# Performance work log

Measured on AMD Instinct MI355X. Metric: run time of the kernel, lower is better.

The kernel has to match this reference:

```python
import jax, jax.numpy as jnp
import numpy as np

D = 64      # in_feats
OUT = 64    # out_feats
MEM = 4     # mem_size
NREL = 8    # num_rels
N = 20000   # num nodes
E = 50000   # num edges
FF = 16     # dim_feedforward (hardcoded in module)
NH = 4      # nhead (hardcoded)
EPS = 1e-5  # LayerNorm eps (torch default)


def _ln(x, w, b):
    m = x.mean(-1, keepdims=True)
    v = ((x - m) ** 2).mean(-1, keepdims=True)
    return (x - m) * jax.lax.rsqrt(v + EPS) * w + b


def _enc(x, Wqkv, bqkv, Wo, bo, W1, b1, W2, b2, ln1w, ln1b, ln2w, ln2b):
    # torch TransformerEncoderLayer, batch_first, post-norm, eval mode, no padding mask (all-zero mask)
    B, S, d = x.shape
    dh = d // NH
    qkv = x @ Wqkv.T + bqkv
    q, k, v = jnp.split(qkv, 3, axis=-1)
    q = q.reshape(B, S, NH, dh)
    k = k.reshape(B, S, NH, dh)
    v = v.reshape(B, S, NH, dh)
    att = jax.nn.softmax(jnp.einsum('bqhd,bkhd->bhqk', q, k) / jnp.sqrt(jnp.float32(dh)), axis=-1)
    o = jnp.einsum('bhqk,bkhd->bqhd', att, v).reshape(B, S, d) @ Wo.T + bo
    x = _ln(x + o, ln1w, ln1b)
    ff = jax.nn.relu(x @ W1.T + b1) @ W2.T + b2
    return _ln(x + ff, ln2w, ln2b)


def setup_inputs() -> dict:
    key = jax.random.key(0)
    ks = jax.random.split(key, 16)
    s = 0.05
    inp = {
        'feat': jax.random.normal(ks[0], (N, D), jnp.float32),
        'src_idx': jax.random.randint(ks[1], (E,), 0, N),
        'dst_idx': jax.random.randint(ks[2], (E,), 0, N),
        'etype': jax.random.randint(ks[3], (E,), 0, NREL),
        'Wqkv': jax.random.normal(ks[4], (3 * D, D), jnp.float32) * s,
        'bqkv': jnp.zeros((3 * D,), jnp.float32),
        'Wo': jax.random.normal(ks[5], (D, D), jnp.float32) * s,
        'bo': jnp.zeros((D,), jnp.float32),
        'W1': jax.random.normal(ks[6], (FF, D), jnp.float32) * s,
        'b1': jnp.zeros((FF,), jnp.float32),
        'W2': jax.random.normal(ks[7], (D, FF), jnp.float32) * s,
        'b2': jnp.zeros((D,), jnp.float32),
        'ln1w': jnp.ones((D,), jnp.float32),
        'ln1b': jnp.zeros((D,), jnp.float32),
        'ln2w': jnp.ones((D,), jnp.float32),
        'ln2b': jnp.zeros((D,), jnp.float32),
        'Wc': jax.random.normal(ks[8], (MEM, D), jnp.float32) * s,
        'bc': jnp.zeros((MEM,), jnp.float32),
        'CLS': jax.random.normal(ks[9], (MEM, D), jnp.float32),
        'SEP': jax.random.normal(ks[10], (D,), jnp.float32),
        'Wm': jax.random.normal(ks[11], (OUT * D, D), jnp.float32) * s,
        'h_bias': jnp.zeros((OUT,), jnp.float32),
    }
    return inp


def reference(feat, src_idx, dst_idx, etype, Wqkv, bqkv, Wo, bo, W1, b1, W2, b2,
              ln1w, ln1b, ln2w, ln2b, Wc, bc, CLS, SEP, Wm, h_bias):
    enc_args = (Wqkv, bqkv, Wo, bo, W1, b1, W2, b2, ln1w, ln1b, ln2w, ln2b)

    def cls_pass(s_, d_):
        # run the shared encoder MEM times with a different CLS token; the math
        # is identical for every relation type, so no per-etype partition needed
        B = s_.shape[0]
        outs = []
        mem = jnp.zeros((B, D), s_.dtype)
        for i in range(MEM):
            cls = jnp.broadcast_to(CLS[i], (B, D))[:, None, :]
            sep = jnp.broadcast_to(SEP, (B, D))[:, None, :]
            seq = jnp.concatenate([cls, s_[:, None, :], sep, d_[:, None, :]], axis=1)  # [B,4,D]
            t = _enc(seq, *enc_args)[:, 0, :]
            outs.append(t)
            mem = mem + t
        return mem, jnp.stack(outs)  # [B,D], [MEM,B,D]

    src = feat[src_idx]  # [E,D]
    dst = feat[dst_idx]
    mem_emb, tmps = cls_pass(src, dst)
    cat_all = tmps @ Wc.T + bc               # [MEM,E,MEM]
    w = (mem_emb @ Wm.T).reshape(E, OUT, D)  # per-edge hypernetwork weight
    msg = jnp.einsum('eoi,ei->eo', w, src)   # [E,OUT]

    # dgl fn.mean aggregation over destination nodes (0 for isolated nodes)
    cnt = jax.ops.segment_sum(jnp.ones((E,), msg.dtype), dst_idx, num_segments=N)
    agg = jax.ops.segment_sum(msg, dst_idx, num_segments=N)
    node_rep = jnp.where(cnt[:, None] > 0, agg / jnp.maximum(cnt, 1.0)[:, None], 0.0)
    node_rep = node_rep + h_bias

    # self loop (same hypernetwork path over every node)
    mem_s, _ = cls_pass(feat, feat)
    hs = (mem_s @ Wm.T).reshape(N, OUT, D)
    node_rep = node_rep + jnp.einsum('noi,ni->no', hs, feat)

    # reconstruct torch concat order of category/label: outer loop etype, inner loop mem idx
    et = etype.astype(jnp.int32)
    counts = jax.ops.segment_sum(jnp.ones((E,), jnp.int32), etype, num_segments=NREL)
    start = jnp.concatenate([jnp.zeros((1,), jnp.int32), jnp.cumsum(counts)[:-1].astype(jnp.int32)])
    order = jnp.argsort(etype, stable=True)
    rank = jnp.zeros((E,), jnp.int32).at[order].set(jnp.arange(E, dtype=jnp.int32) - start[et[order]])
    base = start[et] * MEM + rank                                            # [E]
    pos = base[None, :] + jnp.arange(MEM, dtype=jnp.int32)[:, None] * counts[et][None, :]  # [MEM,E]
    category = jnp.zeros((MEM * E, MEM), cat_all.dtype).at[pos.reshape(-1)].set(cat_all.reshape(-1, MEM))
    label = jnp.zeros((MEM * E,), jnp.int32).at[pos.reshape(-1)].set(
        jnp.repeat(jnp.arange(MEM, dtype=jnp.int32), E))
    return node_rep, label, category
```

## Files before the change

kernel.cpp:

```cpp
#include <hip/hip_runtime.h>
#include <hip/hip_bf16.h>

typedef float f32x4_t __attribute__((ext_vector_type(4)));
typedef short bf16x8_t __attribute__((ext_vector_type(8)));

#define MFMA(a, b, c) __builtin_amdgcn_mfma_f32_16x16x32_bf16(a, b, c, 0, 0, 0)

#define C_Q0   0
#define C_S00  256
#define C_S02  272
#define C_VCLS 288
#define C_VSEP 544

__device__ __forceinline__ short f2bf(float x) {
    return (short)__builtin_bit_cast(unsigned short, __float2bfloat16(x));
}
__device__ __forceinline__ float bf2f(short s) {
    return __builtin_bit_cast(float, ((unsigned)(unsigned short)s) << 16);
}
__device__ __forceinline__ float head_sum16(float v) {
#pragma unroll
    for (int off = 1; off < 16; off <<= 1) v += __shfl_xor(v, off, 64);
    return v;
}

__global__ void k_prep(const float* __restrict__ Wo, const float* __restrict__ Wqkv,
                       const float* __restrict__ W1, const float* __restrict__ W2,
                       const float* __restrict__ Wm, const float* __restrict__ Wc,
                       const float* __restrict__ bqkv,
                       const float* __restrict__ CLS, const float* __restrict__ SEP,
                       const int* __restrict__ etype, const int* __restrict__ dst,
                       short* __restrict__ Bpack, short* __restrict__ WoP,
                       short* __restrict__ WkvP, short* __restrict__ W1P,
                       short* __restrict__ W2P, short* __restrict__ WcP,
                       float* __restrict__ consts,
                       short* __restrict__ WqkP, float* __restrict__ bqk,
                       int* __restrict__ hist, int* __restrict__ cnt, int E)
{
    int bx = blockIdx.x;
    if (bx < 136) {
        int tid = bx * 256 + threadIdx.x;
        short tmp[8];
        if (tid < 32768) {
            int u = tid, lane = u & 63, nt = (u >> 6) & 3, kstep = u >> 8;
            int o = nt * 16 + (lane & 15);
            int kb = kstep * 32 + (lane >> 4) * 8;
#pragma unroll
            for (int t = 0; t < 8; t++) { int k = kb + t; tmp[t] = f2bf(Wm[(o * 64 + (k >> 6)) * 64 + (k & 63)]); }
            *(bf16x8_t*)&Bpack[(size_t)u * 8] = *(bf16x8_t*)tmp;
        } else if (tid < 33280) {
            int u = tid - 32768, lane = u & 63, nt = (u >> 6) & 3, kstep = u >> 8;
            int o = nt * 16 + (lane & 15), kb = kstep * 32 + (lane >> 4) * 8;
#pragma unroll
            for (int t = 0; t < 8; t++) tmp[t] = f2bf(Wo[o * 64 + kb + t]);
            *(bf16x8_t*)&WoP[(size_t)u * 8] = *(bf16x8_t*)tmp;
        } else if (tid < 34304) {
            int u = tid - 33280, lane = u & 63, nt = (u >> 6) & 7, kstep = u >> 9;
            int col = nt * 16 + (lane & 15), kb = kstep * 32 + (lane >> 4) * 8;
            int row = 64 + col;
#pragma unroll
            for (int t = 0; t < 8; t++) tmp[t] = f2bf(Wqkv[row * 64 + kb + t]);
            *(bf16x8_t*)&WkvP[(size_t)u * 8] = *(bf16x8_t*)tmp;
        } else if (tid < 34432) {
            int u = tid - 34304, lane = u & 63, kstep = u >> 6;
            int f = lane & 15, kb = kstep * 32 + (lane >> 4) * 8;
#pragma unroll
            for (int t = 0; t < 8; t++) tmp[t] = f2bf(W1[f * 64 + kb + t]);
            *(bf16x8_t*)&W1P[(size_t)u * 8] = *(bf16x8_t*)tmp;
        } else if (tid < 34688) {
            int u = tid - 34432, lane = u & 63, nt = u >> 6;
            int o = nt * 16 + (lane & 15), kb = (lane >> 4) * 8;
#pragma unroll
            for (int t = 0; t < 8; t++) { int k = kb + t; tmp[t] = (k < 16) ? f2bf(W2[o * 16 + k]) : (short)0; }
            *(bf16x8_t*)&W2P[(size_t)u * 8] = *(bf16x8_t*)tmp;
        } else if (tid < 34816) {
            int u = tid - 34688, lane = u & 63, kstep = u >> 6;
            int m = lane & 15, kb = kstep * 32 + (lane >> 4) * 8;
#pragma unroll
            for (int t = 0; t < 8; t++) tmp[t] = (m < 4) ? f2bf(Wc[m * 64 + kb + t]) : (short)0;
            *(bf16x8_t*)&WcP[(size_t)u * 8] = *(bf16x8_t*)tmp;
        }
    } else if (bx == 136) {
        if (threadIdx.x < 64) {
            int lane = threadIdx.x;
            float ksep = bqkv[64 + lane], vsep = bqkv[128 + lane];
            for (int c = 0; c < 64; c++) {
                float sc = SEP[c];
                ksep += Wqkv[(64 + lane) * 64 + c] * sc;
                vsep += Wqkv[(128 + lane) * 64 + c] * sc;
            }
            consts[C_VSEP + lane] = vsep;
            for (int i = 0; i < 4; i++) {
                float q0 = bqkv[lane], kcls = bqkv[64 + lane], vcls = bqkv[128 + lane];
                for (int c = 0; c < 64; c++) {
                    float cc = CLS[i * 64 + c];
                    q0   += Wqkv[lane * 64 + c] * cc;
                    kcls += Wqkv[(64 + lane) * 64 + c] * cc;
                    vcls += Wqkv[(128 + lane) * 64 + c] * cc;
                }
                consts[C_Q0 + i * 64 + lane] = q0;
                consts[C_VCLS + i * 64 + lane] = vcls;
                float p00 = head_sum16(q0 * kcls) * 0.25f;
                float p02 = head_sum16(q0 * ksep) * 0.25f;
                if ((lane & 15) == 0) {
                    consts[C_S00 + i * 4 + (lane >> 4)] = p00;
                    consts[C_S02 + i * 4 + (lane >> 4)] = p02;
                }
            }
        }
    } else if (bx == 137) {
        __shared__ float q0s[4][64];
        __shared__ float wqk[16][64];
        int tid = threadIdx.x;
        {
            int i = tid >> 6, c = tid & 63;
            float q0 = bqkv[c];
            for (int c2 = 0; c2 < 64; c2++)
                q0 += Wqkv[c * 64 + c2] * CLS[i * 64 + c2];
            q0s[i][c] = q0;
        }
        __syncthreads();
#pragma unroll
        for (int q = 0; q < 4; q++) {
            int idx = tid * 4 + q;
            int ih = idx >> 6, k = idx & 63;
            int ii = ih & 3, hh = ih >> 2;
            float s = 0.f;
#pragma unroll
            for (int u = 0; u < 16; u++)
                s += q0s[ii][hh * 16 + u] * Wqkv[(64 + hh * 16 + u) * 64 + k];
            wqk[ih][k] = 0.25f * s;
        }
        __syncthreads();
        if (tid < 128) {
            int kstep = tid >> 6, lane = tid & 63;
            short tmp[8];
#pragma unroll
            for (int t = 0; t < 8; t++)
                tmp[t] = f2bf(wqk[lane & 15][kstep * 32 + (lane >> 4) * 8 + t]);
            *(bf16x8_t*)&WqkP[(size_t)(kstep * 64 + lane) * 8] = *(bf16x8_t*)tmp;
        } else if (tid < 144) {
            int ihh = tid - 128, ii = ihh & 3, hh = ihh >> 2;
            float s = 0.f;
#pragma unroll
            for (int u = 0; u < 16; u++)
                s += q0s[ii][hh * 16 + u] * bqkv[64 + hh * 16 + u];
            bqk[ihh] = 0.25f * s;
        }
    } else {
        __shared__ int h[8];
        int chunk = bx - 138;
        int tid = threadIdx.x;
        if (tid < 8) h[tid] = 0;
        __syncthreads();
        int e = chunk * 256 + tid;
        if (e < E) {
            atomicAdd(&h[etype[e]], 1);
            atomicAdd(&cnt[dst[e]], 1);
        }
        __syncthreads();
        if (tid < 8) hist[chunk * 8 + tid] = h[tid];
    }
}

__global__ __launch_bounds__(256) void k_kv(const float* __restrict__ feat,
        const short* __restrict__ WkvP, const short* __restrict__ WqkP,
        const float* __restrict__ bqkv, const float* __restrict__ bqk,
        float* __restrict__ vnode, float* __restrict__ qs, int N,
        const int* __restrict__ hist, int* __restrict__ chunkoff,
        int* __restrict__ startg, int* __restrict__ countsg, int nch, int KB)
{
    if ((int)blockIdx.x == KB) {
        if (threadIdx.x < 64) {
            int lane = threadIdx.x;
            int g = lane & 7, seg = lane >> 3;
            int per = (nch + 7) / 8;
            int c0 = seg * per, c1 = c0 + per; if (c1 > nch) c1 = nch;
            int sum = 0;
            for (int c = c0; c < c1; c++) sum += hist[c * 8 + g];
            int pre = 0, tot = 0;
#pragma unroll
            for (int s2 = 0; s2 < 8; s2++) {
                int v = __shfl(sum, s2 * 8 + g, 64);
                tot += v;
                if (s2 < seg) pre += v;
            }
            int run = pre;
            for (int c = c0; c < c1; c++) { chunkoff[c * 8 + g] = run; run += hist[c * 8 + g]; }
            if (seg == 0) {
                countsg[g] = tot;
                int sg = 0;
#pragma unroll
                for (int g2 = 0; g2 < 8; g2++) { int v = __shfl(tot, g2, 64); if (g2 < g) sg += v; }
                startg[g] = sg;
            }
        }
        return;
    }
    __shared__ __align__(16) short sA[64 * 72];
    int tid = threadIdx.x, lane = tid & 63, w = tid >> 6;
    int l15 = lane & 15, lh = lane >> 4;
    int base = blockIdx.x * 64;
#pragma unroll
    for (int rr = 0; rr < 16; rr++) {
        int row = w * 16 + rr;
        int n = base + row; n = n < N ? n : N - 1;
        sA[row * 72 + lane] = f2bf(feat[(size_t)n * 64 + lane]);
    }
    __syncthreads();
    const bf16x8_t* bp = (const bf16x8_t*)WkvP;
    bf16x8_t bv0 = bp[(0 * 8 + 4 + w) * 64 + lane];
    bf16x8_t bv1 = bp[(1 * 8 + 4 + w) * 64 + lane];
    bf16x8_t bq0 = ((const bf16x8_t*)WqkP)[lane];
    bf16x8_t bq1 = ((const bf16x8_t*)WqkP)[64 + lane];
    int kof = lh * 8;
    int col = w * 16 + l15;
    float biasv = bqkv[128 + col];
    float bqv = bqk[l15];
#pragma unroll
    for (int rt = 0; rt < 4; rt++) {
        bf16x8_t a0 = *(const bf16x8_t*)&sA[(rt * 16 + l15) * 72 + kof];
        bf16x8_t a1 = *(const bf16x8_t*)&sA[(rt * 16 + l15) * 72 + 32 + kof];
        f32x4_t av = {0.f, 0.f, 0.f, 0.f};
        av = MFMA(a0, bv0, av); av = MFMA(a1, bv1, av);
#pragma unroll
        for (int r = 0; r < 4; r++) {
            int n = base + rt * 16 + lh * 4 + r;
            if (n < N) vnode[(size_t)n * 64 + col] = av[r] + biasv;
        }
        if (w == 0) {
            f32x4_t aq = {0.f, 0.f, 0.f, 0.f};
            aq = MFMA(a0, bq0, aq); aq = MFMA(a1, bq1, aq);
#pragma unroll
            for (int r = 0; r < 4; r++) {
                int n = base + rt * 16 + lh * 4 + r;
                if (n < N) qs[(size_t)n * 16 + l15] = aq[r] + bqv;
            }
        }
    }
}

struct EncW {
    const float* consts; const float* CLS; const float* bo;
    const float* b1; const float* b2;
    const float* ln1w; const float* ln1b; const float* ln2w; const float* ln2b;
    const short* WoP; const short* W1P; const short* W2P; const short* WcP;
    const float* bc;
};

__global__ __launch_bounds__(256) void k_enc(const int* __restrict__ src_idx,
        const int* __restrict__ dst_idx,
        const float* __restrict__ vnode, const float* __restrict__ qs, EncW W,
        float* __restrict__ mem_out, float* __restrict__ cat_out, int E, int M)
{
    __shared__ __align__(16) short sA[64 * 72];
    __shared__ __align__(16) short sF[64 * 40];
    int tid = threadIdx.x, lane = tid & 63, w = tid >> 6;
    int l15 = lane & 15, lh = lane >> 4;
    int base = blockIdx.x * 16;

#pragma unroll
    for (int z = 0; z < 4; z++) {
        int zz = z * 64 + lane;
        sF[(w * 16 + (zz >> 4)) * 40 + 16 + (zz & 15)] = 0;
    }

    float attc[4], esum0[4];
#pragma unroll
    for (int i = 0; i < 4; i++) {
        float e0 = __expf(W.consts[C_S00 + i * 4 + lh]);
        float e2 = __expf(W.consts[C_S02 + i * 4 + lh]);
        attc[i]  = e0 * W.consts[C_VCLS + i * 64 + lane] + e2 * W.consts[C_VSEP + lane];
        esum0[i] = e0 + e2;
    }

#pragma unroll
    for (int el = 0; el < 4; el++) {
        int eloc = w * 4 + el;
        int ge = base + eloc; int gc = ge < M ? ge : M - 1;
        int s, d;
        if (gc < E) { s = src_idx[gc]; d = dst_idx[gc]; }
        else        { s = gc - E; d = s; }
        float vs_ = vnode[(size_t)s * 64 + lane];
        float vd  = vnode[(size_t)d * 64 + lane];
        float4 qh_s = *(const float4*)&qs[(size_t)s * 16 + lh * 4];
        float4 qh_d = *(const float4*)&qs[(size_t)d * 16 + lh * 4];
        float qsv[4] = {qh_s.x, qh_s.y, qh_s.z, qh_s.w};
        float qdv[4] = {qh_d.x, qh_d.y, qh_d.z, qh_d.w};
#pragma unroll
        for (int i = 0; i < 4; i++) {
            float e1 = __expf(qsv[i]), e3 = __expf(qdv[i]);
            float inv = 1.0f / (esum0[i] + e1 + e3);
            float att = (attc[i] + e1 * vs_ + e3 * vd) * inv;
            sA[(eloc * 4 + i) * 72 + lane] = f2bf(att);
        }
    }

    int arow = (w * 16 + l15) * 72;
    int kof = lh * 8;

    const bf16x8_t* bpo = (const bf16x8_t*)W.WoP;
    f32x4_t ac0 = {0.f,0.f,0.f,0.f}, ac1 = ac0, ac2 = ac0, ac3 = ac0;
#pragma unroll
    for (int kstep = 0; kstep < 2; kstep++) {
        bf16x8_t a = *(const bf16x8_t*)&sA[arow + kstep * 32 + kof];
        ac0 = MFMA(a, bpo[(kstep * 4 + 0) * 64 + lane], ac0);
        ac1 = MFMA(a, bpo[(kstep * 4 + 1) * 64 + lane], ac1);
        ac2 = MFMA(a, bpo[(kstep * 4 + 2) * 64 + lane], ac2);
        ac3 = MFMA(a, bpo[(kstep * 4 + 3) * 64 + lane], ac3);
    }

    float x[4][4], y[4][4];
#pragma unroll
    for (int r = 0; r < 4; r++) { x[0][r] = ac0[r]; x[1][r] = ac1[r]; x[2][r] = ac2[r]; x[3][r] = ac3[r]; }
    float lw1[4], lb1[4];
#pragma unroll
    for (int nt = 0; nt < 4; nt++) {
        float b = W.bo[nt * 16 + l15];
        lw1[nt] = W.ln1w[nt * 16 + l15]; lb1[nt] = W.ln1b[nt * 16 + l15];
#pragma unroll
        for (int r = 0; r < 4; r++) x[nt][r] += b + W.CLS[r * 64 + nt * 16 + l15];
    }
#pragma unroll
    for (int r = 0; r < 4; r++) {
        float sm = head_sum16(x[0][r] + x[1][r] + x[2][r] + x[3][r]);
        float mu = sm * 0.015625f;
        float vv = 0.f;
#pragma unroll
        for (int nt = 0; nt < 4; nt++) { float dd = x[nt][r] - mu; vv = fmaf(dd, dd, vv); }
        vv = head_sum16(vv);
        float rs = rsqrtf(vv * 0.015625f + 1e-5f);
#pragma unroll
        for (int nt = 0; nt < 4; nt++) y[nt][r] = (x[nt][r] - mu) * rs * lw1[nt] + lb1[nt];
    }
#pragma unroll
    for (int nt = 0; nt < 4; nt++)
#pragma unroll
        for (int r = 0; r < 4; r++)
            sA[(w * 16 + lh * 4 + r) * 72 + nt * 16 + l15] = f2bf(y[nt][r]);

    const bf16x8_t* bp1 = (const bf16x8_t*)W.W1P;
    f32x4_t fa = {0.f,0.f,0.f,0.f};
#pragma unroll
    for (int kstep = 0; kstep < 2; kstep++) {
        bf16x8_t a = *(const bf16x8_t*)&sA[arow + kstep * 32 + kof];
        fa = MFMA(a, bp1[kstep * 64 + lane], fa);
    }
    float b1v = W.b1[l15];
#pragma unroll
    for (int r = 0; r < 4; r++)
        sF[(w * 16 + lh * 4 + r) * 40 + l15] = f2bf(fmaxf(fa[r] + b1v, 0.f));

    const bf16x8_t* bp2 = (const bf16x8_t*)W.W2P;
    bf16x8_t af = *(const bf16x8_t*)&sF[(w * 16 + l15) * 40 + kof];
    f32x4_t z0 = {0.f,0.f,0.f,0.f}, z1 = z0, z2 = z0, z3 = z0;
    z0 = MFMA(af, bp2[0 * 64 + lane], z0);
    z1 = MFMA(af, bp2[1 * 64 + lane], z1);
    z2 = MFMA(af, bp2[2 * 64 + lane], z2);
    z3 = MFMA(af, bp2[3 * 64 + lane], z3);

    float t[4][4];
#pragma unroll
    for (int r = 0; r < 4; r++) { x[0][r] = z0[r]; x[1][r] = z1[r]; x[2][r] = z2[r]; x[3][r] = z3[r]; }
    float lw2[4], lb2[4];
#pragma unroll
    for (int nt = 0; nt < 4; nt++) {
        float b = W.b2[nt * 16 + l15];
        lw2[nt] = W.ln2w[nt * 16 + l15]; lb2[nt] = W.ln2b[nt * 16 + l15];
#pragma unroll
        for (int r = 0; r < 4; r++) x[nt][r] += b + y[nt][r];
    }
#pragma unroll
    for (int r = 0; r < 4; r++) {
        float sm = head_sum16(x[0][r] + x[1][r] + x[2][r] + x[3][r]);
        float mu = sm * 0.015625f;
        float vv = 0.f;
#pragma unroll
        for (int nt = 0; nt < 4; nt++) { float dd = x[nt][r] - mu; vv = fmaf(dd, dd, vv); }
        vv = head_sum16(vv);
        float rs = rsqrtf(vv * 0.015625f + 1e-5f);
#pragma unroll
        for (int nt = 0; nt < 4; nt++) t[nt][r] = (x[nt][r] - mu) * rs * lw2[nt] + lb2[nt];
    }

    int eloc = w * 4 + lh, ge = base + eloc;

    if (base < E) {
#pragma unroll
        for (int nt = 0; nt < 4; nt++)
#pragma unroll
            for (int r = 0; r < 4; r++)
                sA[(w * 16 + lh * 4 + r) * 72 + nt * 16 + l15] = f2bf(t[nt][r]);
        const bf16x8_t* bpc = (const bf16x8_t*)W.WcP;
        f32x4_t ca = {0.f,0.f,0.f,0.f};
#pragma unroll
        for (int kstep = 0; kstep < 2; kstep++) {
            bf16x8_t a = *(const bf16x8_t*)&sA[arow + kstep * 32 + kof];
            ca = MFMA(a, bpc[kstep * 64 + lane], ca);
        }
        if (l15 < 4 && ge < E) {
            float bcv = W.bc[l15];
#pragma unroll
            for (int r = 0; r < 4; r++)
                cat_out[((size_t)r * E + ge) * 4 + l15] = ca[r] + bcv;
        }
    }

    if (ge < M) {
#pragma unroll
        for (int nt = 0; nt < 4; nt++)
            mem_out[(size_t)ge * 64 + nt * 16 + l15] = t[nt][0] + t[nt][1] + t[nt][2] + t[nt][3];
    }
}

__global__ __launch_bounds__(256, 3) void k_hyper(
        const float* __restrict__ feat, const int* __restrict__ src_idx,
        const int* __restrict__ dst_idx, const float* __restrict__ memall,
        const short* __restrict__ Bpack,
        float* __restrict__ agg, float* __restrict__ selfm, int E, int M)
{
    __shared__ short xsT[64 * 132];
    __shared__ __align__(16) short sB[2][8192];
    int tid = threadIdx.x, lane = tid & 63, w = tid >> 6;
    int l15 = lane & 15, lh = lane >> 4, koff = lh * 8;
    int base = blockIdx.x * 128;

    const bf16x8_t* bp = (const bf16x8_t*)Bpack;

    auto stage = [&](int c, int buf) {
#pragma unroll
        for (int jj = 0; jj < 4; ++jj) {
            int j = w * 4 + jj;
            int il_ic = j >> 3, q = j & 7;
            const short* src = (const short*)(bp + (size_t)(c * 2 + il_ic) * 512
                                              + (q >> 2) * 256 + (q & 3) * 64 + lane);
            short* dst = &sB[buf][j * 512];
            __builtin_amdgcn_global_load_lds(
                (const __attribute__((address_space(1))) void*)src,
                (__attribute__((address_space(3))) void*)dst, 16, 0, 0);
        }
    };

    stage(0, 0);

    for (int rr = 0; rr < 32; ++rr) {
        int row = w * 32 + rr, gr = base + row;
        float xv = 0.f;
        if (gr < M) {
            int xi = gr < E ? src_idx[gr] : gr - E;
            xv = feat[(size_t)xi * 64 + lane];
        }
        xsT[lane * 132 + row] = f2bf(xv);
    }

    bf16x8_t am[2][2];
#pragma unroll
    for (int tt = 0; tt < 2; ++tt) {
        int gr = base + w * 32 + tt * 16 + l15;
        const float* mp = memall + (size_t)(gr < M ? gr : 0) * 64 + koff;
#pragma unroll
        for (int kk = 0; kk < 2; ++kk)
#pragma unroll
            for (int t = 0; t < 8; ++t)
                am[tt][kk][t] = f2bf(mp[kk * 32 + t]);
    }

    f32x4_t out[2][4];
#pragma unroll
    for (int tt = 0; tt < 2; ++tt)
#pragma unroll
        for (int nt = 0; nt < 4; ++nt) out[tt][nt] = (f32x4_t){0.f, 0.f, 0.f, 0.f};
    const f32x4_t ZERO = {0.f, 0.f, 0.f, 0.f};

    int xrow0 = w * 32 + lh * 4;

    int cur = 0;
    for (int c = 0; c < 32; ++c) {
        asm volatile("s_waitcnt vmcnt(0)" ::: "memory");
        __builtin_amdgcn_s_barrier();
        if (c + 1 < 32) stage(c + 1, cur ^ 1);
#pragma unroll
        for (int ic = 0; ic < 2; ++ic) {
            int i = c * 2 + ic;
            unsigned long long xw0 = *(const unsigned long long*)&xsT[i * 132 + xrow0];
            unsigned long long xw1 = *(const unsigned long long*)&xsT[i * 132 + xrow0 + 16];
            float x0[4], x1[4];
            {
                unsigned lo0 = (unsigned)xw0, hi0 = (unsigned)(xw0 >> 32);
                unsigned lo1 = (unsigned)xw1, hi1 = (unsigned)(xw1 >> 32);
                x0[0] = __builtin_bit_cast(float, lo0 << 16);
                x0[1] = __builtin_bit_cast(float, lo0 & 0xffff0000u);
                x0[2] = __builtin_bit_cast(float, hi0 << 16);
                x0[3] = __builtin_bit_cast(float, hi0 & 0xffff0000u);
                x1[0] = __builtin_bit_cast(float, lo1 << 16);
                x1[1] = __builtin_bit_cast(float, lo1 & 0xffff0000u);
                x1[2] = __builtin_bit_cast(float, hi1 << 16);
                x1[3] = __builtin_bit_cast(float, hi1 & 0xffff0000u);
            }
            const bf16x8_t* bfr = (const bf16x8_t*)&sB[cur][ic * 4096];
            f32x4_t P0[4], P1[4];
            __builtin_amdgcn_s_setprio(1);
#pragma unroll
            for (int nt = 0; nt < 4; ++nt) {
                bf16x8_t B0 = bfr[nt * 64 + lane];
                bf16x8_t B1 = bfr[(4 + nt) * 64 + lane];
                P0[nt] = MFMA(am[0][0], B0, ZERO);
                P1[nt] = MFMA(am[1][0], B0, ZERO);
                P0[nt] = MFMA(am[0][1], B1, P0[nt]);
                P1[nt] = MFMA(am[1][1], B1, P1[nt]);
            }
            __builtin_amdgcn_s_setprio(0);
#pragma unroll
            for (int nt = 0; nt < 4; ++nt)
#pragma unroll
                for (int r = 0; r < 4; ++r) {
                    out[0][nt][r] = fmaf(x0[r], P0[nt][r], out[0][nt][r]);
                    out[1][nt][r] = fmaf(x1[r], P1[nt][r], out[1][nt][r]);
                }
        }
        cur ^= 1;
    }

#pragma unroll
    for (int tt = 0; tt < 2; ++tt) {
        int orow = w * 32 + tt * 16 + lh * 4;
        int di[4];
#pragma unroll
        for (int r = 0; r < 4; ++r) {
            int grow = base + orow + r;
            di[r] = (grow < E) ? dst_idx[grow] : 0;
        }
#pragma unroll
        for (int nt = 0; nt < 4; ++nt) {
            int o = nt * 16 + l15;
#pragma unroll
            for (int r = 0; r < 4; ++r) {
                int grow = base + orow + r;
                if (grow < M) {
                    float v = out[tt][nt][r];
                    if (grow < E) atomicAdd(&agg[(size_t)di[r] * 64 + o], v);
                    else selfm[(size_t)(grow - E) * 64 + o] = v;
                }
            }
        }
    }
}

__global__ __launch_bounds__(256) void k_finsc(
        const float* __restrict__ agg, const int* __restrict__ cnt,
        const float* __restrict__ selfm, const float* __restrict__ h_bias,
        float* __restrict__ outp, int N,
        const int* __restrict__ etype, const float* __restrict__ cat_all,
        const int* __restrict__ chunkoff, const int* __restrict__ startg,
        const int* __restrict__ countsg,
        float* __restrict__ out_label, float* __restrict__ out_cat, int E, int FB)
{
    if ((int)blockIdx.x < FB) {
        int t = blockIdx.x * 256 + threadIdx.x;
        if (t < N * 64) {
            int n = t >> 6, o = t & 63;
            int c = cnt[n];
            float av = (c > 0) ? agg[t] / (float)c : 0.f;
            outp[t] = av + h_bias[o] + selfm[t];
        }
    } else {
        __shared__ int wc[4][8];
        int tid = threadIdx.x, lane = tid & 63, w = tid >> 6;
        int chunk = blockIdx.x - FB;
        int e = chunk * 256 + w * 64 + lane;
        int et = (e < E) ? etype[e] : -1;
        unsigned long long mk[8];
#pragma unroll
        for (int g = 0; g < 8; g++) mk[g] = __ballot(et == g);
        if (lane < 8) wc[w][lane] = (int)__popcll(mk[lane]);
        __syncthreads();
        if (et >= 0) {
            unsigned long long lt = (1ull << lane) - 1ull;
            int myr = chunkoff[chunk * 8 + et] + (int)__popcll(mk[et] & lt);
#pragma unroll
            for (int w2 = 0; w2 < 4; w2++) if (w2 < w) myr += wc[w2][et];
            int sg = startg[et], cg = countsg[et];
            size_t pbase = (size_t)sg * 4 + myr;
#pragma unroll
            for (int i = 0; i < 4; i++) {
                size_t pos = pbase + (size_t)i * cg;
                out_label[pos] = (float)i;
                const float* ca = &cat_all[((size_t)i * E + e) * 4];
                float4 cv = {ca[0], ca[1], ca[2], ca[3]};
                *(float4*)&out_cat[pos * 4] = cv;
            }
        }
    }
}

extern "C" void kernel_launch(void* const* d_in, const int* in_sizes, int n_in,
                              void* d_out, int out_size, void* d_ws, size_t ws_size,
                              hipStream_t stream)
{
    const float* feat    = (const float*)d_in[0];
    const int*   src_idx = (const int*)d_in[1];
    const int*   dst_idx = (const int*)d_in[2];
    const int*   etype   = (const int*)d_in[3];
    const float* Wqkv    = (const float*)d_in[4];
    const float* bqkv    = (const float*)d_in[5];
    const float* Wo      = (const float*)d_in[6];
    const float* bo      = (const float*)d_in[7];
    const float* W1      = (const float*)d_in[8];
    const float* b1      = (const float*)d_in[9];
    const float* W2      = (const float*)d_in[10];
    const float* b2      = (const float*)d_in[11];
    const float* ln1w    = (const float*)d_in[12];
    const float* ln1b    = (const float*)d_in[13];
    const float* ln2w    = (const float*)d_in[14];
    const float* ln2b    = (const float*)d_in[15];
    const float* Wc      = (const float*)d_in[16];
    const float* bc      = (const float*)d_in[17];
    const float* CLS     = (const float*)d_in[18];
    const float* SEP     = (const float*)d_in[19];
    const float* Wm      = (const float*)d_in[20];
    const float* h_bias  = (const float*)d_in[21];

    const int N = in_sizes[0] / 64;
    const int E = in_sizes[1];
    const int M = E + N;
    const int NCH = (E + 255) / 256;
    const int FB = (N * 64 + 255) / 256;
    const int KB = (N + 63) / 64;

    float* ws = (float*)d_ws;
    size_t off = 0;
    auto alloc = [&](size_t n) { float* p = ws + off; off += (n + 63) & ~(size_t)63; return p; };
    float* qs      = alloc((size_t)N * 16);
    float* vnode   = alloc((size_t)N * 64);
    float* mem_all = alloc((size_t)M * 64);
    float* cat_all = alloc((size_t)E * 16);
    float* agg     = alloc((size_t)N * 64 + N);
    int*   cnt     = (int*)(agg + (size_t)N * 64);
    float* selfm   = alloc((size_t)N * 64);
    float* consts  = alloc(1024);
    short* Bpack   = (short*)alloc(131072);
    short* WoP     = (short*)alloc(2048);
    short* WkvP    = (short*)alloc(4096);
    short* W1P     = (short*)alloc(512);
    short* W2P     = (short*)alloc(1024);
    short* WcP     = (short*)alloc(512);
    short* WqkP    = (short*)alloc(512);
    float* bqk     = alloc(64);
    int*   hist    = (int*)alloc(NCH * 8);
    int*   chunkoff= (int*)alloc(NCH * 8);
    int*   startg  = (int*)alloc(8);
    int*   countsg = (int*)alloc(8);

    float* out_node  = (float*)d_out;
    float* out_label = out_node + (size_t)N * 64;
    float* out_cat   = out_label + (size_t)4 * E;

    hipMemsetAsync(agg, 0, ((size_t)N * 64 + N) * sizeof(float), stream);

    k_prep<<<138 + NCH, 256, 0, stream>>>(Wo, Wqkv, W1, W2, Wm, Wc, bqkv, CLS, SEP,
                                          etype, dst_idx, Bpack, WoP, WkvP, W1P, W2P, WcP,
                                          consts, WqkP, bqk, hist, cnt, E);

    k_kv<<<KB + 1, 256, 0, stream>>>(feat, WkvP, WqkP, bqkv, bqk, vnode, qs, N,
                                     hist, chunkoff, startg, countsg, NCH, KB);

    EncW W{consts, CLS, bo, b1, b2, ln1w, ln1b, ln2w, ln2b, WoP, W1P, W2P, WcP, bc};

    k_enc<<<(M + 15) / 16, 256, 0, stream>>>(src_idx, dst_idx, vnode, qs, W,
                                             mem_all, cat_all, E, M);

    k_hyper<<<(M + 127) / 128, 256, 0, stream>>>(feat, src_idx, dst_idx, mem_all, Bpack,
                                                 agg, selfm, E, M);

    k_finsc<<<FB + NCH, 256, 0, stream>>>(agg, cnt, selfm, h_bias, out_node, N,
                                          etype, cat_all, chunkoff, startg, countsg,
                                          out_label, out_cat, E, FB);
}
```

Baseline: 138.8 us.

## Split hypernetwork kernel over output tiles with register-resident weights and LDS reduction

The k_hyper kernel now launches four blocks per 128-row tile, one per 16-wide output slice. Each wave keeps its share of the packed hypernetwork weights in registers instead of streaming them through double-buffered LDS. The wave splits the input dimension, and partial sums are reduced across waves through shared memory before the atomic scatter. This removes the per-chunk barriers and LDS staging of the weights and raises parallelism. In exchange, the feat and mem rows are gathered four times, register pressure rises (launch bounds drop to 2), and there is an extra LDS reduction step.

Result: slower. 245.6 us (+76.9%).

```diff
diff --git a/kernel.cpp b/kernel.cpp
--- a/kernel.cpp
+++ b/kernel.cpp
@@ -413,134 +413,93 @@
     }
 }
 
-__global__ __launch_bounds__(256, 3) void k_hyper(
+__global__ __launch_bounds__(256, 2) void k_hyper(
         const float* __restrict__ feat, const int* __restrict__ src_idx,
         const int* __restrict__ dst_idx, const float* __restrict__ memall,
         const short* __restrict__ Bpack,
         float* __restrict__ agg, float* __restrict__ selfm, int E, int M)
 {
     __shared__ short xsT[64 * 132];
-    __shared__ __align__(16) short sB[2][8192];
+    __shared__ __align__(16) short mL[128 * 72];
+    __shared__ float pL[8 * 4 * 4 * 64];
     int tid = threadIdx.x, lane = tid & 63, w = tid >> 6;
-    int l15 = lane & 15, lh = lane >> 4, koff = lh * 8;
-    int base = blockIdx.x * 128;
-
-    const bf16x8_t* bp = (const bf16x8_t*)Bpack;
-
-    auto stage = [&](int c, int buf) {
-#pragma unroll
-        for (int jj = 0; jj < 4; ++jj) {
-            int j = w * 4 + jj;
-            int il_ic = j >> 3, q = j & 7;
-            const short* src = (const short*)(bp + (size_t)(c * 2 + il_ic) * 512
-                                              + (q >> 2) * 256 + (q & 3) * 64 + lane);
-            short* dst = &sB[buf][j * 512];
-            __builtin_amdgcn_global_load_lds(
-                (const __attribute__((address_space(1))) void*)src,
-                (__attribute__((address_space(3))) void*)dst, 16, 0, 0);
-        }
-    };
-
-    stage(0, 0);
+    int l15 = lane & 15, lh = lane >> 4;
+    int bid = blockIdx.x;
+    int otile = bid & 3, rb = bid >> 2;
+    int base = rb * 128;
+    const f32x4_t ZERO = {0.f, 0.f, 0.f, 0.f};
+
+    bf16x8_t B[16][2];
+    {
+        const bf16x8_t* bp = (const bf16x8_t*)Bpack;
+#pragma unroll
+        for (int ii = 0; ii < 16; ++ii) {
+            int ig = w * 16 + ii;
+#pragma unroll
+            for (int jh = 0; jh < 2; ++jh)
+                B[ii][jh] = bp[(size_t)((ig * 2 + jh) * 4 + otile) * 64 + lane];
+        }
+    }
 
     for (int rr = 0; rr < 32; ++rr) {
         int row = w * 32 + rr, gr = base + row;
-        float xv = 0.f;
+        float xv = 0.f, mv = 0.f;
         if (gr < M) {
             int xi = gr < E ? src_idx[gr] : gr - E;
             xv = feat[(size_t)xi * 64 + lane];
+            mv = memall[(size_t)gr * 64 + lane];
         }
         xsT[lane * 132 + row] = f2bf(xv);
-    }
-
-    bf16x8_t am[2][2];
+        mL[row * 72 + lane] = f2bf(mv);
+    }
+    __syncthreads();
+
+    int xrow_l = lh * 4;
+#pragma unroll 2
+    for (int t = 0; t < 8; ++t) {
+        bf16x8_t A0 = *(const bf16x8_t*)&mL[(t * 16 + l15) * 72 + lh * 8];
+        bf16x8_t A1 = *(const bf16x8_t*)&mL[(t * 16 + l15) * 72 + 32 + lh * 8];
+        f32x4_t acc = ZERO;
+#pragma unroll
+        for (int ii = 0; ii < 16; ++ii) {
+            int ig = w * 16 + ii;
+            unsigned long long xw = *(const unsigned long long*)&xsT[ig * 132 + t * 16 + xrow_l];
+            f32x4_t P = MFMA(A0, B[ii][0], ZERO);
+            P = MFMA(A1, B[ii][1], P);
+            unsigned lo = (unsigned)xw, hi = (unsigned)(xw >> 32);
+            float x0 = __builtin_bit_cast(float, lo << 16);
+            float x1 = __builtin_bit_cast(float, lo & 0xffff0000u);
+            float x2 = __builtin_bit_cast(float, hi << 16);
+            float x3 = __builtin_bit_cast(float, hi & 0xffff0000u);
+            acc[0] = fmaf(x0, P[0], acc[0]);
+            acc[1] = fmaf(x1, P[1], acc[1]);
+            acc[2] = fmaf(x2, P[2], acc[2]);
+            acc[3] = fmaf(x3, P[3], acc[3]);
+        }
+#pragma unroll
+        for (int r = 0; r < 4; ++r)
+            pL[((t * 4 + w) * 4 + r) * 64 + lane] = acc[r];
+    }
+    __syncthreads();
+
 #pragma unroll
     for (int tt = 0; tt < 2; ++tt) {
-        int gr = base + w * 32 + tt * 16 + l15;
-        const float* mp = memall + (size_t)(gr < M ? gr : 0) * 64 + koff;
-#pragma unroll
-        for (int kk = 0; kk < 2; ++kk)
-#pragma unroll
-            for (int t = 0; t < 8; ++t)
-                am[tt][kk][t] = f2bf(mp[kk * 32 + t]);
-    }
-
-    f32x4_t out[2][4];
-#pragma unroll
-    for (int tt = 0; tt < 2; ++tt)
-#pragma unroll
-        for (int nt = 0; nt < 4; ++nt) out[tt][nt] = (f32x4_t){0.f, 0.f, 0.f, 0.f};
-    const f32x4_t ZERO = {0.f, 0.f, 0.f, 0.f};
-
-    int xrow0 = w * 32 + lh * 4;
-
-    int cur = 0;
-    for (int c = 0; c < 32; ++c) {
-        asm volatile("s_waitcnt vmcnt(0)" ::: "memory");
-        __builtin_amdgcn_s_barrier();
-        if (c + 1 < 32) stage(c + 1, cur ^ 1);
-#pragma unroll
-        for (int ic = 0; ic < 2; ++ic) {
-            int i = c * 2 + ic;
-            unsigned long long xw0 = *(const unsigned long long*)&xsT[i * 132 + xrow0];
-            unsigned long long xw1 = *(const unsigned long long*)&xsT[i * 132 + xrow0 + 16];
-            float x0[4], x1[4];
-            {
-                unsigned lo0 = (unsigned)xw0, hi0 = (unsigned)(xw0 >> 32);
-                unsigned lo1 = (unsigned)xw1, hi1 = (unsigned)(xw1 >> 32);
-                x0[0] = __builtin_bit_cast(float, lo0 << 16);
-                x0[1] = __builtin_bit_cast(float, lo0 & 0xffff0000u);
-                x0[2] = __builtin_bit_cast(float, hi0 << 16);
-                x0[3] = __builtin_bit_cast(float, hi0 & 0xffff0000u);
-                x1[0] = __builtin_bit_cast(float, lo1 << 16);
-                x1[1] = __builtin_bit_cast(float, lo1 & 0xffff0000u);
-                x1[2] = __builtin_bit_cast(float, hi1 << 16);
-                x1[3] = __builtin_bit_cast(float, hi1 & 0xffff0000u);
-            }
-            const bf16x8_t* bfr = (const bf16x8_t*)&sB[cur][ic * 4096];
-            f32x4_t P0[4], P1[4];
-            __builtin_amdgcn_s_setprio(1);
-#pragma unroll
-            for (int nt = 0; nt < 4; ++nt) {
-                bf16x8_t B0 = bfr[nt * 64 + lane];
-                bf16x8_t B1 = bfr[(4 + nt) * 64 + lane];
-                P0[nt] = MFMA(am[0][0], B0, ZERO);
-                P1[nt] = MFMA(am[1][0], B0, ZERO);
-                P0[nt] = MFMA(am[0][1], B1, P0[nt]);
-                P1[nt] = MFMA(am[1][1], B1, P1[nt]);
-            }
-            __builtin_amdgcn_s_setprio(0);
-#pragma unroll
-            for (int nt = 0; nt < 4; ++nt)
-#pragma unroll
-                for (int r = 0; r < 4; ++r) {
-                    out[0][nt][r] = fmaf(x0[r], P0[nt][r], out[0][nt][r]);
-                    out[1][nt][r] = fmaf(x1[r], P1[nt][r], out[1][nt][r]);
-                }
-        }
-        cur ^= 1;
-    }
-
-#pragma unroll
-    for (int tt = 0; tt < 2; ++tt) {
-        int orow = w * 32 + tt * 16 + lh * 4;
-        int di[4];
+        int t = w * 2 + tt;
+        float s[4];
+#pragma unroll
+        for (int r = 0; r < 4; ++r)
+            s[r] = pL[((t * 4 + 0) * 4 + r) * 64 + lane]
+                 + pL[((t * 4 + 1) * 4 + r) * 64 + lane]
+                 + pL[((t * 4 + 2) * 4 + r) * 64 + lane]
+                 + pL[((t * 4 + 3) * 4 + r) * 64 + lane];
+        int orow = t * 16 + lh * 4;
+        int o = otile * 16 + l15;
 #pragma unroll
         for (int r = 0; r < 4; ++r) {
             int grow = base + orow + r;
-            di[r] = (grow < E) ? dst_idx[grow] : 0;
-        }
-#pragma unroll
-        for (int nt = 0; nt < 4; ++nt) {
-            int o = nt * 16 + l15;
-#pragma unroll
-            for (int r = 0; r < 4; ++r) {
-                int grow = base + orow + r;
-                if (grow < M) {
-                    float v = out[tt][nt][r];
-                    if (grow < E) atomicAdd(&agg[(size_t)di[r] * 64 + o], v);
-                    else selfm[(size_t)(grow - E) * 64 + o] = v;
-                }
+            if (grow < M) {
+                if (grow < E) atomicAdd(&agg[(size_t)dst_idx[grow] * 64 + o], s[r]);
+                else selfm[(size_t)(grow - E) * 64 + o] = s[r];
             }
         }
     }
@@ -669,8 +628,8 @@
     k_enc<<<(M + 15) / 16, 256, 0, stream>>>(src_idx, dst_idx, vnode, qs, W,
                                              mem_all, cat_all, E, M);
 
-    k_hyper<<<(M + 127) / 128, 256, 0, stream>>>(feat, src_idx, dst_idx, mem_all, Bpack,
-                                                 agg, selfm, E, M);
+    k_hyper<<<((M + 127) / 128) * 4, 256, 0, stream>>>(feat, src_idx, dst_idx, mem_all, Bpack,
+                                                       agg, selfm, E, M);
 
     k_finsc<<<FB + NCH, 256, 0, stream>>>(agg, cnt, selfm, h_bias, out_node, N,
                                           etype, cat_all, chunkoff, startg, countsg,
```
